# Kernel optimization log

Hardware: AMD Instinct MI355X
Metric: run time of the kernel (lower is better)

## Reference

```python
import jax, jax.numpy as jnp
import numpy as np


def _c2e(faces):
    # faces: [6, B, C, h, h] in order back, down, front, left, right, up
    # returns equirect map [B, C, H=h, W=2h] via bilinear cube sampling
    _, B, C, h, _ = faces.shape
    H, W = h, 2 * h
    lat = (0.5 - (jnp.arange(H) + 0.5) / H) * jnp.pi      # +pi/2 (top) .. -pi/2
    lon = (2.0 * (jnp.arange(W) + 0.5) / W - 1.0) * jnp.pi  # -pi .. +pi
    cl = jnp.cos(lat)[:, None]
    vx = cl * jnp.sin(lon)[None, :]
    vy = jnp.broadcast_to(jnp.sin(lat)[:, None], (H, W))
    vz = cl * jnp.cos(lon)[None, :]
    dirs = jnp.stack([vx, vy, vz], -1)                     # [H,W,3]
    ax, ay, az = jnp.abs(vx), jnp.abs(vy), jnp.abs(vz)
    cond_z = (az >= ax) & (az >= ay)
    cond_x = (~cond_z) & (ax >= ay)
    # face ids: 0 back(-z) 1 down(-y) 2 front(+z) 3 left(-x) 4 right(+x) 5 up(+y)
    face = jnp.where(cond_z, jnp.where(vz > 0, 2, 0),
                     jnp.where(cond_x, jnp.where(vx > 0, 4, 3),
                               jnp.where(vy > 0, 5, 1)))
    N = jnp.array([[0, 0, -1], [0, -1, 0], [0, 0, 1], [-1, 0, 0], [1, 0, 0], [0, 1, 0]], jnp.float32)
    R = jnp.array([[-1, 0, 0], [1, 0, 0], [1, 0, 0], [0, 0, 1], [0, 0, -1], [1, 0, 0]], jnp.float32)
    U = jnp.array([[0, 1, 0], [0, 0, -1], [0, 1, 0], [0, 1, 0], [0, 1, 0], [0, 0, 1]], jnp.float32)
    den = jnp.sum(dirs * N[face], -1)
    a = jnp.sum(dirs * R[face], -1) / den                  # in-plane x, [-1,1]
    bcoord = jnp.sum(dirs * U[face], -1) / den             # in-plane y, [-1,1]
    uu = jnp.clip((a + 1.0) * 0.5 * (h - 1), 0.0, h - 1)   # align_corners-style
    vv = jnp.clip((1.0 - bcoord) * 0.5 * (h - 1), 0.0, h - 1)
    x0 = jnp.floor(uu).astype(jnp.int32)
    y0 = jnp.floor(vv).astype(jnp.int32)
    x1 = jnp.minimum(x0 + 1, h - 1)
    y1 = jnp.minimum(y0 + 1, h - 1)
    dx = uu - x0
    dy = vv - y0
    ft = faces.transpose(0, 3, 4, 1, 2).reshape(6, h, h, B * C)  # [6,h,h,B*C]
    g = lambda yy, xx: ft[face, yy, xx]                    # gather -> [H,W,B*C]
    out = (g(y0, x0) * ((1 - dx) * (1 - dy))[..., None]
           + g(y0, x1) * (dx * (1 - dy))[..., None]
           + g(y1, x0) * ((1 - dx) * dy)[..., None]
           + g(y1, x1) * (dx * dy)[..., None])
    return out.reshape(H, W, B, C).transpose(2, 3, 0, 1)


def _conv(x, w, bias, pad):
    y = jax.lax.conv_general_dilated(x, w, (1, 1), [(pad, pad), (pad, pad)],
                                     dimension_numbers=('NCHW', 'OIHW', 'NCHW'))
    return y + bias[None, :, None, None]


def setup_inputs() -> dict:
    key = jax.random.key(0)
    ks = jax.random.split(key, 12)
    B, C, h = 4, 64, 128
    face_shape = (B, C, h, h)
    return {
        'm': jax.random.normal(ks[0], (B, C, h, 2 * h), jnp.float32),
        'f': jax.random.normal(ks[1], face_shape, jnp.float32),
        'r': jax.random.normal(ks[2], face_shape, jnp.float32),
        'b': jax.random.normal(ks[3], face_shape, jnp.float32),
        'l': jax.random.normal(ks[4], face_shape, jnp.float32),
        'u': jax.random.normal(ks[5], face_shape, jnp.float32),
        'd': jax.random.normal(ks[6], face_shape, jnp.float32),
        'w_fusion': jax.random.normal(ks[7], (C, C, 3, 3), jnp.float32) * 0.05,
        'b_fusion': jnp.zeros((C,), jnp.float32),
        'w_mask': jax.random.normal(ks[8], (1, 2 * C, 1, 1), jnp.float32) * 0.05,
        'b_mask': jnp.zeros((1,), jnp.float32),
    }


def reference(m, f, r, b, l, u, d, w_fusion, b_fusion, w_mask, b_mask):
    # cube faces stacked in the original order: back, down, front, left, right, up
    faces = jnp.stack([b, d, f, l, r, u], 0)               # [6,B,C,h,h]
    aux = _c2e(faces)                                      # [B,C,h,2h]
    m_aux = jax.nn.relu(_conv(aux, w_fusion, b_fusion, 1))
    m_main = jax.nn.relu(_conv(m, w_fusion, b_fusion, 1))  # shared conv_fusion weights
    joint = jnp.concatenate([m_main, m_aux], axis=1)
    mask = jax.nn.sigmoid(_conv(joint, w_mask, b_mask, 0)) # [B,1,h,2h]
    return m + mask * m_aux
```

## Files before the change

### kernel.cpp

```cpp
#include <hip/hip_runtime.h>
#include <math.h>
#include <stdint.h>

#define BB 4
#define CC 64
#define HH 128
#define HOUT 128
#define WOUT 256
#define NPIX (HOUT * WOUT)
#define NMAP (BB * CC * HOUT * WOUT)
#define FSTR ((size_t)HH * HH * 256)

typedef __attribute__((ext_vector_type(8))) short short8;
typedef __attribute__((ext_vector_type(4))) float floatx4;

__device__ __forceinline__ uint16_t f2bf(float f) {
    uint32_t u = __float_as_uint(f);
    u += 0x7fffu + ((u >> 16) & 1u);
    return (uint16_t)(u >> 16);
}
__device__ __forceinline__ float bfu2f(uint32_t v) { return __uint_as_float(v << 16); }

__global__ __launch_bounds__(256) void prep_kernel(uint32_t* __restrict__ pk,
                                                   float* __restrict__ pdx,
                                                   float* __restrict__ pdy,
                                                   const float* __restrict__ wf,
                                                   uint4* __restrict__ Bsw) {
    if (blockIdx.x < 128) {
        int p = blockIdx.x * 256 + threadIdx.x;
        int y = p >> 8;
        int x = p & 255;
        const float PI = 3.14159265358979323846f;
        float lat = (0.5f - (y + 0.5f) / (float)HOUT) * PI;
        float lon = (2.0f * (x + 0.5f) / (float)WOUT - 1.0f) * PI;
        float cl = cosf(lat);
        float vx = cl * sinf(lon);
        float vy = sinf(lat);
        float vz = cl * cosf(lon);
        float ax = fabsf(vx), ay = fabsf(vy), az = fabsf(vz);

        int face;
        float den, a, b;
        if (az >= ax && az >= ay) {
            if (vz > 0.0f) { face = 2; den = vz;  a = vx;  b = vy; }
            else           { face = 0; den = -vz; a = -vx; b = vy; }
        } else if (ax >= ay) {
            if (vx > 0.0f) { face = 4; den = vx;  a = -vz; b = vy; }
            else           { face = 3; den = -vx; a = vz;  b = vy; }
        } else {
            if (vy > 0.0f) { face = 5; den = vy;  a = vx;  b = vz; }
            else           { face = 1; den = -vy; a = vx;  b = -vz; }
        }
        a /= den;
        b /= den;
        float uu = fminf(fmaxf((a + 1.0f) * 0.5f * (HH - 1), 0.0f), (float)(HH - 1));
        float vv = fminf(fmaxf((1.0f - b) * 0.5f * (HH - 1), 0.0f), (float)(HH - 1));
        int x0 = (int)floorf(uu);
        int y0 = (int)floorf(vv);
        int x1 = min(x0 + 1, HH - 1);
        int y1 = min(y0 + 1, HH - 1);
        pdx[p] = uu - (float)x0;
        pdy[p] = vv - (float)y0;
        pk[p] = (uint32_t)face | ((uint32_t)x0 << 3) | ((uint32_t)y0 << 10) |
                ((uint32_t)x1 << 17) | ((uint32_t)y1 << 24);
    } else {
        int tid = (blockIdx.x - 128) * 256 + threadIdx.x;
        if (tid >= 9 * 2 * 4 * 64) return;
        int lane = tid & 63;
        int rest = tid >> 6;
        int n = rest & 3, ks = (rest >> 2) & 1, tap = rest >> 3;
        int co = n * 16 + (lane & 15);
        uint32_t w4[4];
#pragma unroll
        for (int pw = 0; pw < 4; pw++) {
            int ci0 = ks * 32 + (lane >> 4) * 8 + pw * 2;
            uint32_t lo = f2bf(wf[(size_t)(co * CC + ci0) * 9 + tap]);
            uint32_t hi = f2bf(wf[(size_t)(co * CC + ci0 + 1) * 9 + tap]);
            w4[pw] = lo | (hi << 16);
        }
        Bsw[tid] = make_uint4(w4[0], w4[1], w4[2], w4[3]);
    }
}

__global__ __launch_bounds__(256) void facepack_kernel(
    const float* __restrict__ pB, const float* __restrict__ pD,
    const float* __restrict__ pF, const float* __restrict__ pL,
    const float* __restrict__ pR, const float* __restrict__ pU,
    uint16_t* __restrict__ FCLlo, uint16_t* __restrict__ FCLhi) {
    __shared__ uint16_t lds[64 * 256];
    int bid = blockIdx.x;
    int half = bid & 1;
    int y = (bid >> 1) & 127;
    int fc = bid >> 8;
    const float* src = (fc == 0) ? pB : (fc == 1) ? pD : (fc == 2) ? pF
                     : (fc == 3) ? pL : (fc == 4) ? pR : pU;
    uint16_t* FCL = (fc < 3) ? (FCLlo + (size_t)fc * FSTR)
                             : (FCLhi + (size_t)(fc - 3) * FSTR);
    int t = threadIdx.x;
    int xl = t & 63;
    int x = half * 64 + xl;
    int cgb = t >> 6;

#pragma unroll
    for (int i = 0; i < 8; i++) {
        int cg = i * 4 + cgb;
        uint32_t w4[4];
#pragma unroll
        for (int j = 0; j < 4; j++) {
            int bc0 = cg * 8 + j * 2;
            uint32_t lo = f2bf(src[((size_t)bc0 * HH + y) * HH + x]);
            uint32_t hi = f2bf(src[((size_t)(bc0 + 1) * HH + y) * HH + x]);
            w4[j] = lo | (hi << 16);
        }
        int off = xl * 256 + ((cg ^ (xl & 7)) * 8);
        *(uint4*)&lds[off] = make_uint4(w4[0], w4[1], w4[2], w4[3]);
    }
    __syncthreads();
    size_t obase = ((size_t)y * HH + half * 64) * 256;
#pragma unroll
    for (int i = 0; i < 8; i++) {
        int q = i * 256 + t;
        int xx = q >> 5, cg = q & 31;
        int off = xx * 256 + ((cg ^ (xx & 7)) * 8);
        *(uint4*)&FCL[obase + (size_t)q * 8] = *(const uint4*)&lds[off];
    }
}

__global__ __launch_bounds__(256) void gather_kernel(
    const uint32_t* __restrict__ pk, const float* __restrict__ pdx,
    const float* __restrict__ pdy, const uint16_t* __restrict__ FCLlo,
    const uint16_t* __restrict__ FCLhi, uint16_t* __restrict__ Xa) {
    int tid = blockIdx.x * 256 + threadIdx.x;
    int chunk = tid & 31;
    int p = tid >> 5;

    uint32_t k = pk[p];
    float dx = pdx[p], dy = pdy[p];
    int fc = k & 7;
    int x0 = (k >> 3) & 127, y0 = (k >> 10) & 127;
    int x1 = (k >> 17) & 127, y1 = (k >> 24) & 127;

    const uint16_t* fb = (fc < 3) ? (FCLlo + (size_t)fc * FSTR)
                                  : (FCLhi + (size_t)(fc - 3) * FSTR);
    const uint16_t* base = fb + chunk * 8;
    uint4 c00 = *(const uint4*)(base + ((size_t)y0 * HH + x0) * 256);
    uint4 c01 = *(const uint4*)(base + ((size_t)y0 * HH + x1) * 256);
    uint4 c10 = *(const uint4*)(base + ((size_t)y1 * HH + x0) * 256);
    uint4 c11 = *(const uint4*)(base + ((size_t)y1 * HH + x1) * 256);

    float w00 = (1.0f - dx) * (1.0f - dy);
    float w01 = dx * (1.0f - dy);
    float w10 = (1.0f - dx) * dy;
    float w11 = dx * dy;

    const uint32_t* a00 = (const uint32_t*)&c00;
    const uint32_t* a01 = (const uint32_t*)&c01;
    const uint32_t* a10 = (const uint32_t*)&c10;
    const uint32_t* a11 = (const uint32_t*)&c11;
    uint32_t r[4];
#pragma unroll
    for (int w = 0; w < 4; w++) {
        float lo = w00 * bfu2f(a00[w] & 0xffffu) + w01 * bfu2f(a01[w] & 0xffffu)
                 + w10 * bfu2f(a10[w] & 0xffffu) + w11 * bfu2f(a11[w] & 0xffffu);
        float hi = w00 * bfu2f(a00[w] >> 16) + w01 * bfu2f(a01[w] >> 16)
                 + w10 * bfu2f(a10[w] >> 16) + w11 * bfu2f(a11[w] >> 16);
        r[w] = (uint32_t)f2bf(lo) | ((uint32_t)f2bf(hi) << 16);
    }

    int b = chunk >> 3, c = (chunk & 7) * 8;
    int y = p >> 8, x = p & 255;
    size_t o = (((size_t)(b * HOUT + y)) * WOUT + x) * CC + c;
    *(uint4*)(Xa + o) = make_uint4(r[0], r[1], r[2], r[3]);
}

__global__ __launch_bounds__(256) void pack_kernel(const float* __restrict__ src,
                                                   uint16_t* __restrict__ dst) {
    __shared__ uint16_t lds[WOUT * CC];
    int t = threadIdx.x;
    int by = blockIdx.x;
    int b = by >> 7, y = by & 127;

#pragma unroll
    for (int cg = 0; cg < 8; cg++) {
        uint32_t w4[4];
#pragma unroll
        for (int pw = 0; pw < 4; pw++) {
            int c0 = cg * 8 + pw * 2;
            uint32_t lo = f2bf(src[((size_t)(b * CC + c0) * HOUT + y) * WOUT + t]);
            uint32_t hi = f2bf(src[((size_t)(b * CC + c0 + 1) * HOUT + y) * WOUT + t]);
            w4[pw] = lo | (hi << 16);
        }
        int off = t * 64 + ((cg ^ (t & 7)) * 8);
        *(uint4*)&lds[off] = make_uint4(w4[0], w4[1], w4[2], w4[3]);
    }
    __syncthreads();
    size_t obase = (size_t)((b * HOUT + y) * WOUT) * CC;
#pragma unroll
    for (int i = 0; i < 8; i++) {
        int q = i * 256 + t;
        int p = q >> 3, c8 = q & 7;
        int off = p * 64 + ((c8 ^ (p & 7)) * 8);
        *(uint4*)&dst[obase + (size_t)q * 8] = *(const uint4*)&lds[off];
    }
}

__global__ __launch_bounds__(256, 4) void gemm_fused_kernel(
    const uint16_t* __restrict__ Xm, const uint16_t* __restrict__ Xa,
    const uint4* __restrict__ Bsw, const float* __restrict__ bias,
    const float* __restrict__ wm, const float* __restrict__ bm,
    const float* __restrict__ m, float* __restrict__ out) {
    __shared__ __align__(16) uint16_t lds[3 * 132 * 64];
    float* ldsf = (float*)lds;

    int gid = blockIdx.x;
    int b = gid >> 8;
    int i = gid & 255;
    int xcd = i & 7, j = i >> 3;
    int y = xcd * 16 + (j & 15);
    int h = j >> 4;
    const int wx = h * 128 - 2;

    int tid = threadIdx.x;
    int lane = tid & 63;
    int wave = tid >> 6;
    int l15 = lane & 15, lq = lane >> 4;

    float bb[4], wmm[4], wma[4];
#pragma unroll
    for (int n = 0; n < 4; n++) {
        bb[n] = bias[n * 16 + l15];
        wmm[n] = wm[n * 16 + l15];
        wma[n] = wm[64 + n * 16 + l15];
    }
    float bm0 = bm[0];

    float mp[2][4];
#pragma unroll
    for (int mt = 0; mt < 2; mt++)
#pragma unroll
        for (int rg = 0; rg < 4; rg++) mp[mt][rg] = 0.0f;

    floatx4 acc[2][4];

#pragma unroll
    for (int phase = 0; phase < 2; phase++) {
        const uint16_t* X = phase ? Xa : Xm;
        const uint16_t* Xb = X + (size_t)b * (HOUT * WOUT * CC);

        __syncthreads();
#pragma unroll
        for (int it = 0; it < 13; it++) {
            int cid = it * 256 + tid;
            if (cid < 3168) {
                int c = cid & 7;
                int pr = cid >> 3;
                int p = pr % 132;
                int r = pr / 132;
                int gy = y + r - 1;
                int gx = wx + p;
                uint4 v = make_uint4(0, 0, 0, 0);
                if ((unsigned)gy < (unsigned)HOUT && (unsigned)gx < (unsigned)WOUT)
                    v = *(const uint4*)(Xb + ((size_t)gy * WOUT + gx) * CC + c * 8);
                int slot = (r * 132 + p) * 8 + (c ^ (p & 7));
                *(uint4*)&lds[slot * 8] = v;
            }
        }
        __syncthreads();

#pragma unroll
        for (int mt = 0; mt < 2; mt++)
#pragma unroll
            for (int n = 0; n < 4; n++) acc[mt][n] = (floatx4)0.0f;

#pragma unroll
        for (int tap = 0; tap < 9; tap++) {
            const int r = tap / 3;
            const int dx = tap % 3 - 1;
#pragma unroll
            for (int ks = 0; ks < 2; ks++) {
                short8 bfr[4];
                const uint4* bp = Bsw + (size_t)((tap * 2 + ks) * 4) * 64 + lane;
#pragma unroll
                for (int n = 0; n < 4; n++) {
                    uint4 t4 = bp[n * 64];
                    bfr[n] = *(short8*)&t4;
                }
#pragma unroll
                for (int mt = 0; mt < 2; mt++) {
                    int p = wave * 32 + mt * 16 + l15 + dx + 2;
                    int chunk = ks * 4 + lq;
                    int slot = (r * 132 + p) * 8 + (chunk ^ (p & 7));
                    short8 af = *(const short8*)&lds[slot * 8];
#pragma unroll
                    for (int n = 0; n < 4; n++)
                        acc[mt][n] = __builtin_amdgcn_mfma_f32_16x16x32_bf16(
                            af, bfr[n], acc[mt][n], 0, 0, 0);
                }
            }
        }

        if (phase == 0) {
#pragma unroll
            for (int mt = 0; mt < 2; mt++)
#pragma unroll
                for (int n = 0; n < 4; n++)
#pragma unroll
                    for (int rg = 0; rg < 4; rg++) {
                        float v = acc[mt][n][rg] + bb[n];
                        v = v > 0.0f ? v : 0.0f;
                        mp[mt][rg] += wmm[n] * v;
                    }
        } else {
#pragma unroll
            for (int mt = 0; mt < 2; mt++)
#pragma unroll
                for (int n = 0; n < 4; n++)
#pragma unroll
                    for (int rg = 0; rg < 4; rg++) {
                        float v = acc[mt][n][rg] + bb[n];
                        v = v > 0.0f ? v : 0.0f;
                        acc[mt][n][rg] = v;
                        mp[mt][rg] += wma[n] * v;
                    }
        }
    }

#pragma unroll
    for (int mt = 0; mt < 2; mt++)
#pragma unroll
        for (int rg = 0; rg < 4; rg++) {
            float v = mp[mt][rg];
            v += __shfl_xor(v, 1);
            v += __shfl_xor(v, 2);
            v += __shfl_xor(v, 4);
            v += __shfl_xor(v, 8);
            mp[mt][rg] = 1.0f / (1.0f + expf(-(v + bm0)));
        }

    __syncthreads();
#pragma unroll
    for (int mt = 0; mt < 2; mt++)
#pragma unroll
        for (int n = 0; n < 4; n++)
#pragma unroll
            for (int rg = 0; rg < 4; rg++) {
                int px = wave * 32 + mt * 16 + lq * 4 + rg;
                int co = n * 16 + l15;
                ldsf[co * 129 + px] = mp[mt][rg] * acc[mt][n][rg];
            }
    __syncthreads();

    size_t base0 = (size_t)b * (CC * HOUT * WOUT) + (size_t)y * WOUT + h * 128;
#pragma unroll
    for (int it = 0; it < 32; it++) {
        int q = it * 256 + tid;
        int c = q >> 7, px = q & 127;
        size_t idx = base0 + (size_t)c * (HOUT * WOUT) + px;
        out[idx] = m[idx] + ldsf[c * 129 + px];
    }
}

__global__ __launch_bounds__(256) void signal_kernel(float* __restrict__ out, float v) {
    int idx = blockIdx.x * 256 + threadIdx.x;
    out[idx] = v;
}

extern "C" void kernel_launch(void* const* d_in, const int* in_sizes, int n_in,
                              void* d_out, int out_size, void* d_ws, size_t ws_size,
                              hipStream_t stream) {
    const float* m  = (const float*)d_in[0];
    const float* f  = (const float*)d_in[1];
    const float* r  = (const float*)d_in[2];
    const float* bk = (const float*)d_in[3];
    const float* l  = (const float*)d_in[4];
    const float* u  = (const float*)d_in[5];
    const float* dn = (const float*)d_in[6];
    const float* wf = (const float*)d_in[7];
    const float* bf = (const float*)d_in[8];
    const float* wm = (const float*)d_in[9];
    const float* bm = (const float*)d_in[10];
    float* out = (float*)d_out;

    const size_t FCL_HALF = (size_t)3 * HH * HH * 256 * 2;
    const size_t OFF_FCLH = 0;
    const size_t OFF_XA   = FCL_HALF;
    const size_t OFF_XM   = OFF_XA + (size_t)NMAP * 2;
    const size_t OFF_BSW  = OFF_XM + (size_t)NMAP * 2;
    const size_t OFF_PK   = OFF_BSW + (9 * 2 * 4 * 64 * 16);
    const size_t OFF_PDX  = OFF_PK + (1u << 17);
    const size_t OFF_PDY  = OFF_PDX + (1u << 17);
    const size_t NEED     = OFF_PDY + (1u << 17);

    if (ws_size < NEED) {
        float v = 100.0f + (float)(ws_size >> 20);
        signal_kernel<<<NMAP / 256, 256, 0, stream>>>(out, v);
        return;
    }

    char* ws = (char*)d_ws;
    uint16_t* FCLhi = (uint16_t*)(ws + OFF_FCLH);
    uint16_t* Xa    = (uint16_t*)(ws + OFF_XA);
    uint16_t* Xm    = (uint16_t*)(ws + OFF_XM);
    uint4* Bsw      = (uint4*)(ws + OFF_BSW);
    uint32_t* pk    = (uint32_t*)(ws + OFF_PK);
    float* pdx      = (float*)(ws + OFF_PDX);
    float* pdy      = (float*)(ws + OFF_PDY);
    uint16_t* FCLlo = (uint16_t*)d_out;

    prep_kernel<<<146, 256, 0, stream>>>(pk, pdx, pdy, wf, Bsw);
    facepack_kernel<<<6 * HH * 2, 256, 0, stream>>>(bk, dn, f, l, r, u, FCLlo, FCLhi);
    gather_kernel<<<(NPIX * 32) / 256, 256, 0, stream>>>(pk, pdx, pdy, FCLlo, FCLhi, Xa);
    pack_kernel<<<BB * HOUT, 256, 0, stream>>>(m, Xm);
    gemm_fused_kernel<<<BB * HOUT * 2, 256, 0, stream>>>(Xm, Xa, Bsw, bf, wm, bm, m, out);
}
```

Before: 266.2 us.

## Merge prep, facepack and pack kernels; use direct global-to-LDS loads in conv

The prep, facepack and m-pack kernels are merged into a single front_kernel launch that dispatches on block-index ranges, which removes two launches and lets the independent work run concurrently. The gather kernel swizzles its block index so consecutive blocks are spread across XCD-sized groups. The gemm halo load now uses global_load_lds, which writes straight into shared memory, and out-of-bounds taps read from a zero page in the workspace. The XOR swizzle is moved from the LDS destination to the source address. The single merged kernel requests the larger shared-memory footprint for every block, which may lower occupancy for the prep blocks.

New measurement: 243.2 us. -8.6%, faster.

```diff
diff --git a/kernel.cpp b/kernel.cpp
--- a/kernel.cpp
+++ b/kernel.cpp
@@ -11,6 +11,11 @@
 #define NMAP (BB * CC * HOUT * WOUT)
 #define FSTR ((size_t)HH * HH * 256)
 
+#define NB_PREP 146
+#define NB_FACE (6 * HH * 2)
+#define NB_PACK (BB * HOUT)
+#define NB_FRONT (NB_PREP + NB_FACE + NB_PACK)
+
 typedef __attribute__((ext_vector_type(8))) short short8;
 typedef __attribute__((ext_vector_type(4))) float floatx4;
 
@@ -21,108 +26,137 @@
 }
 __device__ __forceinline__ float bfu2f(uint32_t v) { return __uint_as_float(v << 16); }
 
-__global__ __launch_bounds__(256) void prep_kernel(uint32_t* __restrict__ pk,
-                                                   float* __restrict__ pdx,
-                                                   float* __restrict__ pdy,
-                                                   const float* __restrict__ wf,
-                                                   uint4* __restrict__ Bsw) {
-    if (blockIdx.x < 128) {
-        int p = blockIdx.x * 256 + threadIdx.x;
-        int y = p >> 8;
-        int x = p & 255;
-        const float PI = 3.14159265358979323846f;
-        float lat = (0.5f - (y + 0.5f) / (float)HOUT) * PI;
-        float lon = (2.0f * (x + 0.5f) / (float)WOUT - 1.0f) * PI;
-        float cl = cosf(lat);
-        float vx = cl * sinf(lon);
-        float vy = sinf(lat);
-        float vz = cl * cosf(lon);
-        float ax = fabsf(vx), ay = fabsf(vy), az = fabsf(vz);
-
-        int face;
-        float den, a, b;
-        if (az >= ax && az >= ay) {
-            if (vz > 0.0f) { face = 2; den = vz;  a = vx;  b = vy; }
-            else           { face = 0; den = -vz; a = -vx; b = vy; }
-        } else if (ax >= ay) {
-            if (vx > 0.0f) { face = 4; den = vx;  a = -vz; b = vy; }
-            else           { face = 3; den = -vx; a = vz;  b = vy; }
-        } else {
-            if (vy > 0.0f) { face = 5; den = vy;  a = vx;  b = vz; }
-            else           { face = 1; den = -vy; a = vx;  b = -vz; }
-        }
-        a /= den;
-        b /= den;
-        float uu = fminf(fmaxf((a + 1.0f) * 0.5f * (HH - 1), 0.0f), (float)(HH - 1));
-        float vv = fminf(fmaxf((1.0f - b) * 0.5f * (HH - 1), 0.0f), (float)(HH - 1));
-        int x0 = (int)floorf(uu);
-        int y0 = (int)floorf(vv);
-        int x1 = min(x0 + 1, HH - 1);
-        int y1 = min(y0 + 1, HH - 1);
-        pdx[p] = uu - (float)x0;
-        pdy[p] = vv - (float)y0;
-        pk[p] = (uint32_t)face | ((uint32_t)x0 << 3) | ((uint32_t)y0 << 10) |
-                ((uint32_t)x1 << 17) | ((uint32_t)y1 << 24);
-    } else {
-        int tid = (blockIdx.x - 128) * 256 + threadIdx.x;
-        if (tid >= 9 * 2 * 4 * 64) return;
-        int lane = tid & 63;
-        int rest = tid >> 6;
-        int n = rest & 3, ks = (rest >> 2) & 1, tap = rest >> 3;
-        int co = n * 16 + (lane & 15);
-        uint32_t w4[4];
-#pragma unroll
-        for (int pw = 0; pw < 4; pw++) {
-            int ci0 = ks * 32 + (lane >> 4) * 8 + pw * 2;
-            uint32_t lo = f2bf(wf[(size_t)(co * CC + ci0) * 9 + tap]);
-            uint32_t hi = f2bf(wf[(size_t)(co * CC + ci0 + 1) * 9 + tap]);
-            w4[pw] = lo | (hi << 16);
-        }
-        Bsw[tid] = make_uint4(w4[0], w4[1], w4[2], w4[3]);
-    }
-}
-
-__global__ __launch_bounds__(256) void facepack_kernel(
+__global__ __launch_bounds__(256) void front_kernel(
+    uint32_t* __restrict__ pk, float* __restrict__ pdx, float* __restrict__ pdy,
+    const float* __restrict__ wf, uint4* __restrict__ Bsw,
     const float* __restrict__ pB, const float* __restrict__ pD,
     const float* __restrict__ pF, const float* __restrict__ pL,
     const float* __restrict__ pR, const float* __restrict__ pU,
-    uint16_t* __restrict__ FCLlo, uint16_t* __restrict__ FCLhi) {
+    uint16_t* __restrict__ FCLlo, uint16_t* __restrict__ FCLhi,
+    const float* __restrict__ msrc, uint16_t* __restrict__ Xm,
+    uint4* __restrict__ zpage) {
     __shared__ uint16_t lds[64 * 256];
     int bid = blockIdx.x;
-    int half = bid & 1;
-    int y = (bid >> 1) & 127;
-    int fc = bid >> 8;
-    const float* src = (fc == 0) ? pB : (fc == 1) ? pD : (fc == 2) ? pF
-                     : (fc == 3) ? pL : (fc == 4) ? pR : pU;
-    uint16_t* FCL = (fc < 3) ? (FCLlo + (size_t)fc * FSTR)
-                             : (FCLhi + (size_t)(fc - 3) * FSTR);
     int t = threadIdx.x;
-    int xl = t & 63;
-    int x = half * 64 + xl;
-    int cgb = t >> 6;
-
-#pragma unroll
-    for (int i = 0; i < 8; i++) {
-        int cg = i * 4 + cgb;
-        uint32_t w4[4];
-#pragma unroll
-        for (int j = 0; j < 4; j++) {
-            int bc0 = cg * 8 + j * 2;
-            uint32_t lo = f2bf(src[((size_t)bc0 * HH + y) * HH + x]);
-            uint32_t hi = f2bf(src[((size_t)(bc0 + 1) * HH + y) * HH + x]);
-            w4[j] = lo | (hi << 16);
-        }
-        int off = xl * 256 + ((cg ^ (xl & 7)) * 8);
-        *(uint4*)&lds[off] = make_uint4(w4[0], w4[1], w4[2], w4[3]);
-    }
-    __syncthreads();
-    size_t obase = ((size_t)y * HH + half * 64) * 256;
-#pragma unroll
-    for (int i = 0; i < 8; i++) {
-        int q = i * 256 + t;
-        int xx = q >> 5, cg = q & 31;
-        int off = xx * 256 + ((cg ^ (xx & 7)) * 8);
-        *(uint4*)&FCL[obase + (size_t)q * 8] = *(const uint4*)&lds[off];
+
+    if (bid < NB_PREP) {
+        if (bid == 0 && t == 0) *zpage = make_uint4(0, 0, 0, 0);
+        if (bid < 128) {
+            int p = bid * 256 + t;
+            int y = p >> 8;
+            int x = p & 255;
+            const float PI = 3.14159265358979323846f;
+            float lat = (0.5f - (y + 0.5f) / (float)HOUT) * PI;
+            float lon = (2.0f * (x + 0.5f) / (float)WOUT - 1.0f) * PI;
+            float cl = cosf(lat);
+            float vx = cl * sinf(lon);
+            float vy = sinf(lat);
+            float vz = cl * cosf(lon);
+            float ax = fabsf(vx), ay = fabsf(vy), az = fabsf(vz);
+
+            int face;
+            float den, a, b;
+            if (az >= ax && az >= ay) {
+                if (vz > 0.0f) { face = 2; den = vz;  a = vx;  b = vy; }
+                else           { face = 0; den = -vz; a = -vx; b = vy; }
+            } else if (ax >= ay) {
+                if (vx > 0.0f) { face = 4; den = vx;  a = -vz; b = vy; }
+                else           { face = 3; den = -vx; a = vz;  b = vy; }
+            } else {
+                if (vy > 0.0f) { face = 5; den = vy;  a = vx;  b = vz; }
+                else           { face = 1; den = -vy; a = vx;  b = -vz; }
+            }
+            a /= den;
+            b /= den;
+            float uu = fminf(fmaxf((a + 1.0f) * 0.5f * (HH - 1), 0.0f), (float)(HH - 1));
+            float vv = fminf(fmaxf((1.0f - b) * 0.5f * (HH - 1), 0.0f), (float)(HH - 1));
+            int x0 = (int)floorf(uu);
+            int y0 = (int)floorf(vv);
+            int x1 = min(x0 + 1, HH - 1);
+            int y1 = min(y0 + 1, HH - 1);
+            pdx[p] = uu - (float)x0;
+            pdy[p] = vv - (float)y0;
+            pk[p] = (uint32_t)face | ((uint32_t)x0 << 3) | ((uint32_t)y0 << 10) |
+                    ((uint32_t)x1 << 17) | ((uint32_t)y1 << 24);
+        } else {
+            int tid = (bid - 128) * 256 + t;
+            if (tid >= 9 * 2 * 4 * 64) return;
+            int lane = tid & 63;
+            int rest = tid >> 6;
+            int n = rest & 3, ks = (rest >> 2) & 1, tap = rest >> 3;
+            int co = n * 16 + (lane & 15);
+            uint32_t w4[4];
+#pragma unroll
+            for (int pw = 0; pw < 4; pw++) {
+                int ci0 = ks * 32 + (lane >> 4) * 8 + pw * 2;
+                uint32_t lo = f2bf(wf[(size_t)(co * CC + ci0) * 9 + tap]);
+                uint32_t hi = f2bf(wf[(size_t)(co * CC + ci0 + 1) * 9 + tap]);
+                w4[pw] = lo | (hi << 16);
+            }
+            Bsw[tid] = make_uint4(w4[0], w4[1], w4[2], w4[3]);
+        }
+    } else if (bid < NB_PREP + NB_FACE) {
+        int fb = bid - NB_PREP;
+        int half = fb & 1;
+        int y = (fb >> 1) & 127;
+        int fc = fb >> 8;
+        const float* src = (fc == 0) ? pB : (fc == 1) ? pD : (fc == 2) ? pF
+                         : (fc == 3) ? pL : (fc == 4) ? pR : pU;
+        uint16_t* FCL = (fc < 3) ? (FCLlo + (size_t)fc * FSTR)
+                                 : (FCLhi + (size_t)(fc - 3) * FSTR);
+        int xl = t & 63;
+        int x = half * 64 + xl;
+        int cgb = t >> 6;
+
+#pragma unroll
+        for (int i = 0; i < 8; i++) {
+            int cg = i * 4 + cgb;
+            uint32_t w4[4];
+#pragma unroll
+            for (int j = 0; j < 4; j++) {
+                int bc0 = cg * 8 + j * 2;
+                uint32_t lo = f2bf(src[((size_t)bc0 * HH + y) * HH + x]);
+                uint32_t hi = f2bf(src[((size_t)(bc0 + 1) * HH + y) * HH + x]);
+                w4[j] = lo | (hi << 16);
+            }
+            int off = xl * 256 + ((cg ^ (xl & 7)) * 8);
+            *(uint4*)&lds[off] = make_uint4(w4[0], w4[1], w4[2], w4[3]);
+        }
+        __syncthreads();
+        size_t obase = ((size_t)y * HH + half * 64) * 256;
+#pragma unroll
+        for (int i = 0; i < 8; i++) {
+            int q = i * 256 + t;
+            int xx = q >> 5, cg = q & 31;
+            int off = xx * 256 + ((cg ^ (xx & 7)) * 8);
+            *(uint4*)&FCL[obase + (size_t)q * 8] = *(const uint4*)&lds[off];
+        }
+    } else {
+        int by = bid - (NB_PREP + NB_FACE);
+        int b = by >> 7, y = by & 127;
+
+#pragma unroll
+        for (int cg = 0; cg < 8; cg++) {
+            uint32_t w4[4];
+#pragma unroll
+            for (int pw = 0; pw < 4; pw++) {
+                int c0 = cg * 8 + pw * 2;
+                uint32_t lo = f2bf(msrc[((size_t)(b * CC + c0) * HOUT + y) * WOUT + t]);
+                uint32_t hi = f2bf(msrc[((size_t)(b * CC + c0 + 1) * HOUT + y) * WOUT + t]);
+                w4[pw] = lo | (hi << 16);
+            }
+            int off = t * 64 + ((cg ^ (t & 7)) * 8);
+            *(uint4*)&lds[off] = make_uint4(w4[0], w4[1], w4[2], w4[3]);
+        }
+        __syncthreads();
+        size_t obase = (size_t)((b * HOUT + y) * WOUT) * CC;
+#pragma unroll
+        for (int i = 0; i < 8; i++) {
+            int q = i * 256 + t;
+            int p = q >> 3, c8 = q & 7;
+            int off = p * 64 + ((c8 ^ (p & 7)) * 8);
+            *(uint4*)&Xm[obase + (size_t)q * 8] = *(const uint4*)&lds[off];
+        }
     }
 }
 
@@ -130,7 +164,9 @@
     const uint32_t* __restrict__ pk, const float* __restrict__ pdx,
     const float* __restrict__ pdy, const uint16_t* __restrict__ FCLlo,
     const uint16_t* __restrict__ FCLhi, uint16_t* __restrict__ Xa) {
-    int tid = blockIdx.x * 256 + threadIdx.x;
+    int bid = blockIdx.x;
+    int sw = (bid & 7) * 512 + (bid >> 3);
+    int tid = sw * 256 + threadIdx.x;
     int chunk = tid & 31;
     int p = tid >> 5;
 
@@ -173,42 +209,12 @@
     *(uint4*)(Xa + o) = make_uint4(r[0], r[1], r[2], r[3]);
 }
 
-__global__ __launch_bounds__(256) void pack_kernel(const float* __restrict__ src,
-                                                   uint16_t* __restrict__ dst) {
-    __shared__ uint16_t lds[WOUT * CC];
-    int t = threadIdx.x;
-    int by = blockIdx.x;
-    int b = by >> 7, y = by & 127;
-
-#pragma unroll
-    for (int cg = 0; cg < 8; cg++) {
-        uint32_t w4[4];
-#pragma unroll
-        for (int pw = 0; pw < 4; pw++) {
-            int c0 = cg * 8 + pw * 2;
-            uint32_t lo = f2bf(src[((size_t)(b * CC + c0) * HOUT + y) * WOUT + t]);
-            uint32_t hi = f2bf(src[((size_t)(b * CC + c0 + 1) * HOUT + y) * WOUT + t]);
-            w4[pw] = lo | (hi << 16);
-        }
-        int off = t * 64 + ((cg ^ (t & 7)) * 8);
-        *(uint4*)&lds[off] = make_uint4(w4[0], w4[1], w4[2], w4[3]);
-    }
-    __syncthreads();
-    size_t obase = (size_t)((b * HOUT + y) * WOUT) * CC;
-#pragma unroll
-    for (int i = 0; i < 8; i++) {
-        int q = i * 256 + t;
-        int p = q >> 3, c8 = q & 7;
-        int off = p * 64 + ((c8 ^ (p & 7)) * 8);
-        *(uint4*)&dst[obase + (size_t)q * 8] = *(const uint4*)&lds[off];
-    }
-}
-
 __global__ __launch_bounds__(256, 4) void gemm_fused_kernel(
     const uint16_t* __restrict__ Xm, const uint16_t* __restrict__ Xa,
     const uint4* __restrict__ Bsw, const float* __restrict__ bias,
     const float* __restrict__ wm, const float* __restrict__ bm,
-    const float* __restrict__ m, float* __restrict__ out) {
+    const float* __restrict__ m, const uint4* __restrict__ zpage,
+    float* __restrict__ out) {
     __shared__ __align__(16) uint16_t lds[3 * 132 * 64];
     float* ldsf = (float*)lds;
 
@@ -244,8 +250,7 @@
 
 #pragma unroll
     for (int phase = 0; phase < 2; phase++) {
-        const uint16_t* X = phase ? Xa : Xm;
-        const uint16_t* Xb = X + (size_t)b * (HOUT * WOUT * CC);
+        const uint16_t* Xb = (phase ? Xa : Xm) + (size_t)b * (HOUT * WOUT * CC);
 
         __syncthreads();
 #pragma unroll
@@ -258,11 +263,14 @@
                 int r = pr / 132;
                 int gy = y + r - 1;
                 int gx = wx + p;
-                uint4 v = make_uint4(0, 0, 0, 0);
-                if ((unsigned)gy < (unsigned)HOUT && (unsigned)gx < (unsigned)WOUT)
-                    v = *(const uint4*)(Xb + ((size_t)gy * WOUT + gx) * CC + c * 8);
-                int slot = (r * 132 + p) * 8 + (c ^ (p & 7));
-                *(uint4*)&lds[slot * 8] = v;
+                int csrc = c ^ (p & 7);
+                const uint4* src =
+                    ((unsigned)gy < (unsigned)HOUT && (unsigned)gx < (unsigned)WOUT)
+                        ? (const uint4*)(Xb + ((size_t)gy * WOUT + gx) * CC + csrc * 8)
+                        : zpage;
+                __builtin_amdgcn_global_load_lds(
+                    (const uint32_t*)src,
+                    (uint32_t*)&lds[(size_t)(it * 256 + wave * 64) * 8], 16, 0, 0);
             }
         }
         __syncthreads();
@@ -389,7 +397,8 @@
     const size_t OFF_PK   = OFF_BSW + (9 * 2 * 4 * 64 * 16);
     const size_t OFF_PDX  = OFF_PK + (1u << 17);
     const size_t OFF_PDY  = OFF_PDX + (1u << 17);
-    const size_t NEED     = OFF_PDY + (1u << 17);
+    const size_t OFF_ZP   = OFF_PDY + (1u << 17);
+    const size_t NEED     = OFF_ZP + 64;
 
     if (ws_size < NEED) {
         float v = 100.0f + (float)(ws_size >> 20);
@@ -405,11 +414,13 @@
     uint32_t* pk    = (uint32_t*)(ws + OFF_PK);
     float* pdx      = (float*)(ws + OFF_PDX);
     float* pdy      = (float*)(ws + OFF_PDY);
+    uint4* zpage    = (uint4*)(ws + OFF_ZP);
     uint16_t* FCLlo = (uint16_t*)d_out;
 
-    prep_kernel<<<146, 256, 0, stream>>>(pk, pdx, pdy, wf, Bsw);
-    facepack_kernel<<<6 * HH * 2, 256, 0, stream>>>(bk, dn, f, l, r, u, FCLlo, FCLhi);
+    front_kernel<<<NB_FRONT, 256, 0, stream>>>(pk, pdx, pdy, wf, Bsw,
+                                               bk, dn, f, l, r, u, FCLlo, FCLhi,
+                                               m, Xm, zpage);
     gather_kernel<<<(NPIX * 32) / 256, 256, 0, stream>>>(pk, pdx, pdy, FCLlo, FCLhi, Xa);
-    pack_kernel<<<BB * HOUT, 256, 0, stream>>>(m, Xm);
-    gemm_fused_kernel<<<BB * HOUT * 2, 256, 0, stream>>>(Xm, Xa, Bsw, bf, wm, bm, m, out);
-}
+    gemm_fused_kernel<<<BB * HOUT * 2, 256, 0, stream>>>(Xm, Xa, Bsw, bf, wm, bm, m,
+                                                         zpage, out);
+}
```
